# Kernel optimization log

Measured on AMD Instinct MI355X. Metric: run time of the kernel, lower is better.

Reference implementation:

```python
import jax, jax.numpy as jnp
import numpy as np

EPS = 1e-12  # F.normalize eps


def _lstm_dir(x, Wih_d, Whh_d, b_d, reverse):
    # x: [M, dim]; Wih_d/Whh_d: [4*dim, dim]; b_d: [4*dim]
    dim = Whh_d.shape[1]
    def step(carry, xt):
        h, c = carry
        z = xt @ Wih_d.T + h @ Whh_d.T + b_d  # [4*dim]
        i, f, g, o = jnp.split(z, 4)
        i = jax.nn.sigmoid(i); f = jax.nn.sigmoid(f)
        g = jnp.tanh(g); o = jax.nn.sigmoid(o)
        c = f * c + i * g
        h = o * jnp.tanh(c)
        return (h, c), h
    init = (jnp.zeros((dim,), x.dtype), jnp.zeros((dim,), x.dtype))
    _, hs = jax.lax.scan(step, init, x, reverse=reverse)
    return hs  # [M, dim]


def _forward(fingerprints, adjacency, words, emb_fp, emb_word,
             Wg, bg, Wih, Whh, bih, bhh, Wc, bc, Wp, bp, Wo, bo, Wi, bi):
    # ---- GAT over compound graph ----
    xs = emb_fp[fingerprints]  # [N, dim]
    L_gat = Wg.shape[0]
    for i in range(L_gat):
        hs = jax.nn.relu(xs @ Wg[i].T + bg[i])          # [N, dim]
        w = hs @ hs.T                                    # [N, N]
        attn = w * adjacency
        denom = jnp.maximum(jnp.sum(jnp.abs(attn), axis=1, keepdims=True), EPS)
        xs = xs + (attn / denom) @ hs
    x = xs  # compound atom vectors [N, dim]

    # ---- bidirectional LSTM over protein words ----
    wv = emb_word[words]  # [M, dim]
    h_f = _lstm_dir(wv, Wih[0], Whh[0], bih[0] + bhh[0], reverse=False)
    h_b = _lstm_dir(wv, Wih[1], Whh[1], bih[1] + bhh[1], reverse=True)
    xs_rnn = jax.nn.relu(jnp.concatenate([h_f, h_b], axis=1))  # [M, 2*dim]

    # ---- cross attention pooling ----
    h = jax.nn.relu(x @ Wc.T + bc)         # [N, dim]
    hp = jax.nn.relu(xs_rnn @ Wp.T + bp)   # [M, dim]
    weights = h @ hp.T                     # [N, M]
    w_comp = jnp.mean(weights, axis=1)     # [N]  (mean over M)
    w_prot = jnp.mean(weights, axis=0)     # [M]
    y = w_comp[:, None] * h                # [N, dim]
    ys = w_prot[:, None] * hp              # [M, dim]
    compound_vector = jnp.mean(y, axis=0)[None, :]   # [1, dim]
    protein_vector = jnp.mean(ys, axis=0)[None, :]   # [1, dim]

    # ---- output MLP ----
    cat = jnp.concatenate([compound_vector, protein_vector], axis=1)  # [1, 2*dim]
    L_out = Wo.shape[0]
    for j in range(L_out):
        cat = jax.nn.relu(cat @ Wo[j].T + bo[j])
    interaction = cat @ Wi.T + bi  # [1, 2]
    return interaction, weights


def setup_inputs() -> dict:
    key = jax.random.key(0)
    ks = jax.random.split(key, 16)
    N, M, DIM = 4096, 4096, 128
    N_FP, N_WORD = 100000, 10000
    L_GAT, L_OUT = 3, 2
    s = 0.05
    return {
        "fingerprints": jax.random.randint(ks[0], (N,), 0, N_FP),
        "adjacency": jax.random.uniform(ks[1], (N, N), jnp.float32),
        "words": jax.random.randint(ks[2], (M,), 0, N_WORD),
        "emb_fp": jax.random.normal(ks[3], (N_FP, DIM), jnp.float32) * s,
        "emb_word": jax.random.normal(ks[4], (N_WORD, DIM), jnp.float32) * s,
        "Wg": jax.random.normal(ks[5], (L_GAT, DIM, DIM), jnp.float32) * s,
        "bg": jnp.zeros((L_GAT, DIM), jnp.float32),
        "Wih": jax.random.normal(ks[6], (2, 4 * DIM, DIM), jnp.float32) * s,
        "Whh": jax.random.normal(ks[7], (2, 4 * DIM, DIM), jnp.float32) * s,
        "bih": jnp.zeros((2, 4 * DIM), jnp.float32),
        "bhh": jnp.zeros((2, 4 * DIM), jnp.float32),
        "Wc": jax.random.normal(ks[8], (DIM, DIM), jnp.float32) * s,
        "bc": jnp.zeros((DIM,), jnp.float32),
        "Wp": jax.random.normal(ks[9], (DIM, 2 * DIM), jnp.float32) * s,
        "bp": jnp.zeros((DIM,), jnp.float32),
        "Wo": jax.random.normal(ks[10], (L_OUT, 2 * DIM, 2 * DIM), jnp.float32) * s,
        "bo": jnp.zeros((L_OUT, 2 * DIM), jnp.float32),
        "Wi": jax.random.normal(ks[11], (2, 2 * DIM), jnp.float32) * s,
        "bi": jnp.zeros((2,), jnp.float32),
    }


def reference(fingerprints, adjacency, words, emb_fp, emb_word,
              Wg, bg, Wih, Whh, bih, bhh, Wc, bc, Wp, bp, Wo, bo, Wi, bi):
    return _forward(fingerprints, adjacency, words, emb_fp, emb_word,
                    Wg, bg, Wih, Whh, bih, bhh, Wc, bc, Wp, bp, Wo, bo, Wi, bi)
```

## Files before the change

### kernel.cpp

```cpp
#include <hip/hip_runtime.h>
#include <hip/hip_bf16.h>
#include <math.h>

#define DIM 128

typedef float v2f __attribute__((ext_vector_type(2)));
typedef _Float16 v2h __attribute__((ext_vector_type(2)));
typedef _Float16 h8v __attribute__((ext_vector_type(8)));
typedef short s8v __attribute__((ext_vector_type(8)));
typedef float f4v __attribute__((ext_vector_type(4)));

template<int CTRL>
__device__ inline float dpp_movf(float v) {
  int x = __builtin_amdgcn_update_dpp(0, __float_as_int(v), CTRL, 0xF, 0xF, true);
  return __int_as_float(x);
}
template<int CTRL>
__device__ inline float dpp_xadd(float v) { return v + dpp_movf<CTRL>(v); }

__device__ inline float dot8u(uint4 a, uint4 b, float acc) {
#if __has_builtin(__builtin_amdgcn_fdot2)
  acc = __builtin_amdgcn_fdot2(__builtin_bit_cast(v2h, a.x), __builtin_bit_cast(v2h, b.x), acc, false);
  acc = __builtin_amdgcn_fdot2(__builtin_bit_cast(v2h, a.y), __builtin_bit_cast(v2h, b.y), acc, false);
  acc = __builtin_amdgcn_fdot2(__builtin_bit_cast(v2h, a.z), __builtin_bit_cast(v2h, b.z), acc, false);
  acc = __builtin_amdgcn_fdot2(__builtin_bit_cast(v2h, a.w), __builtin_bit_cast(v2h, b.w), acc, false);
#else
  const v2h* pa = (const v2h*)&a; const v2h* pb = (const v2h*)&b;
#pragma unroll
  for (int i = 0; i < 4; ++i) {
    acc += (float)pa[i][0] * (float)pb[i][0];
    acc += (float)pa[i][1] * (float)pb[i][1];
  }
#endif
  return acc;
}

__device__ inline unsigned pk2h(float a, float b) {
  return __builtin_bit_cast(unsigned, __builtin_amdgcn_cvt_pkrtz(a, b));
}
__device__ inline float sigm_fast(float z) {
  return __builtin_amdgcn_rcpf(1.f + __expf(-z));
}
__device__ inline float tanh_fast(float z) {
  float e = __expf(-2.f * z);
  return (1.f - e) * __builtin_amdgcn_rcpf(1.f + e);
}
__device__ inline ushort f2bf(float x) {
  unsigned u = __builtin_bit_cast(unsigned, x);
  return (ushort)((u + 0x7FFFu + ((u >> 16) & 1u)) >> 16);
}
__device__ inline unsigned pk2bf(float a, float b) {
  return (unsigned)f2bf(a) | ((unsigned)f2bf(b) << 16);
}

__global__ void gather_rows(const float* __restrict__ table, const int* __restrict__ idx,
                            float* __restrict__ dst, int n) {
  int i = blockIdx.x * blockDim.x + threadIdx.x;
  int total = n * 32;
  if (i >= total) return;
  int r = i >> 5, c = i & 31;
  const float4* src = (const float4*)table + (size_t)idx[r] * 32 + c;
  ((float4*)dst)[i] = *src;
}
__global__ void gather_rows_wv(const float* __restrict__ table, const int* __restrict__ idx,
                               float* __restrict__ dst, _Float16* __restrict__ dsth, int n) {
  int i = blockIdx.x * blockDim.x + threadIdx.x;
  int total = n * 32;
  if (i >= total) return;
  int r = i >> 5, c = i & 31;
  float4 v = ((const float4*)table)[(size_t)idx[r] * 32 + c];
  ((float4*)dst)[i] = v;
  ((uint2*)dsth)[i] = make_uint2(pk2h(v.x, v.y), pk2h(v.z, v.w));
}

__global__ void conv_f16(const float* __restrict__ src, _Float16* __restrict__ dst, int n4) {
  int i = blockIdx.x * blockDim.x + threadIdx.x;
  if (i >= n4) return;
  float4 v = ((const float4*)src)[i];
  ((uint2*)dst)[i] = make_uint2(pk2h(v.x, v.y), pk2h(v.z, v.w));
}

__global__ void tr_bf16(const ushort* __restrict__ src, ushort* __restrict__ dT, int n) {
  int i = blockIdx.x * blockDim.x + threadIdx.x;
  if (i >= n * DIM) return;
  int r = i >> 7, d = i & 127;
  dT[(size_t)d * n + r] = src[i];
}

template<bool RELU, int OM>
__global__ __launch_bounds__(256) void gemm_nt(
    const float* __restrict__ A, const float* __restrict__ B,
    float* __restrict__ C, ushort* __restrict__ Cb, _Float16* __restrict__ Ch,
    int ldc, int K, const float* __restrict__ bias)
{
  __shared__ float As[64][17];
  __shared__ float Bs[64][17];
  int tid = threadIdx.x;
  int tx = tid & 15, ty = tid >> 4;
  int rowBase = blockIdx.y * 64, colBase = blockIdx.x * 64;
  int lr = tid >> 2, lk = (tid & 3) * 4;
  float acc[4][4] = {};
  for (int k0 = 0; k0 < K; k0 += 16) {
    float4 av = *(const float4*)&A[(size_t)(rowBase + lr) * K + k0 + lk];
    float4 bv = *(const float4*)&B[(size_t)(colBase + lr) * K + k0 + lk];
    As[lr][lk+0]=av.x; As[lr][lk+1]=av.y; As[lr][lk+2]=av.z; As[lr][lk+3]=av.w;
    Bs[lr][lk+0]=bv.x; Bs[lr][lk+1]=bv.y; Bs[lr][lk+2]=bv.z; Bs[lr][lk+3]=bv.w;
    __syncthreads();
#pragma unroll
    for (int kk = 0; kk < 16; ++kk) {
      float a0=As[ty*4+0][kk], a1=As[ty*4+1][kk], a2=As[ty*4+2][kk], a3=As[ty*4+3][kk];
      float b0=Bs[tx*4+0][kk], b1=Bs[tx*4+1][kk], b2=Bs[tx*4+2][kk], b3=Bs[tx*4+3][kk];
      acc[0][0]+=a0*b0; acc[0][1]+=a0*b1; acc[0][2]+=a0*b2; acc[0][3]+=a0*b3;
      acc[1][0]+=a1*b0; acc[1][1]+=a1*b1; acc[1][2]+=a1*b2; acc[1][3]+=a1*b3;
      acc[2][0]+=a2*b0; acc[2][1]+=a2*b1; acc[2][2]+=a2*b2; acc[2][3]+=a2*b3;
      acc[3][0]+=a3*b0; acc[3][1]+=a3*b1; acc[3][2]+=a3*b2; acc[3][3]+=a3*b3;
    }
    __syncthreads();
  }
  int row = rowBase + ty*4, col = colBase + tx*4;
#pragma unroll
  for (int i = 0; i < 4; ++i) {
    float v[4];
#pragma unroll
    for (int j = 0; j < 4; ++j) {
      float x = acc[i][j] + bias[col + j];
      if (RELU) x = fmaxf(x, 0.f);
      v[j] = x;
    }
    size_t base = (size_t)(row + i) * ldc + col;
    if (OM == 1) {
      *(uint2*)&Cb[base] = make_uint2(pk2bf(v[0], v[1]), pk2bf(v[2], v[3]));
    } else {
      float* cp = &C[base];
      *(float2*)cp = make_float2(v[0], v[1]);
      *(float2*)(cp+2) = make_float2(v[2], v[3]);
      if (OM == 2)
        *(uint2*)&Ch[base] = make_uint2(pk2h(v[0], v[1]), pk2h(v[2], v[3]));
    }
  }
}

#define LDT 136
__global__ __launch_bounds__(256) void mfma_nt_adj(
    const ushort* __restrict__ A, const ushort* __restrict__ B,
    ushort* __restrict__ C, int ldc,
    const float* __restrict__ adj, int ldadj)
{
  __shared__ ushort As[128][LDT];
  __shared__ ushort Bs[128][LDT];
  int tid = threadIdx.x;
  int rowBase = blockIdx.y * 128, colBase = blockIdx.x * 128;
#pragma unroll
  for (int it = 0; it < 8; ++it) {
    int c = it * 256 + tid;
    int r = c >> 4, ch = (c & 15) * 8;
    *(uint4*)&As[r][ch] = *(const uint4*)&A[(size_t)(rowBase + r) * DIM + ch];
    *(uint4*)&Bs[r][ch] = *(const uint4*)&B[(size_t)(colBase + r) * DIM + ch];
  }
  __syncthreads();
  int lane = tid & 63;
  int wv = tid >> 6, wr = wv >> 1, wc = wv & 1;
  int lr = lane & 15, lk = (lane >> 4) * 8;
  f4v acc[4][4] = {};
#pragma unroll
  for (int kc = 0; kc < 4; ++kc) {
    s8v a[4], b[4];
#pragma unroll
    for (int i = 0; i < 4; ++i) {
      a[i] = *(const s8v*)&As[wr*64 + i*16 + lr][kc*32 + lk];
      b[i] = *(const s8v*)&Bs[wc*64 + i*16 + lr][kc*32 + lk];
    }
#pragma unroll
    for (int i = 0; i < 4; ++i)
#pragma unroll
      for (int j = 0; j < 4; ++j)
        acc[i][j] = __builtin_amdgcn_mfma_f32_16x16x32_bf16(a[i], b[j], acc[i][j], 0, 0, 0);
  }
  int rsub = (lane >> 4) * 4;
#pragma unroll
  for (int i = 0; i < 4; ++i)
#pragma unroll
    for (int j = 0; j < 4; ++j) {
      int col = colBase + wc*64 + j*16 + lr;
#pragma unroll
      for (int rg = 0; rg < 4; ++rg) {
        int row = rowBase + wr*64 + i*16 + rsub + rg;
        float v = acc[i][j][rg] * adj[(size_t)row * ldadj + col];
        C[(size_t)row * ldc + col] = f2bf(v);
      }
    }
}

__global__ __launch_bounds__(256) void mfma_nt_f32(
    const _Float16* __restrict__ A, const _Float16* __restrict__ B,
    float* __restrict__ C, int ldc)
{
  __shared__ ushort As[128][LDT];
  __shared__ ushort Bs[128][LDT];
  int tid = threadIdx.x;
  int rowBase = blockIdx.y * 128, colBase = blockIdx.x * 128;
#pragma unroll
  for (int it = 0; it < 8; ++it) {
    int c = it * 256 + tid;
    int r = c >> 4, ch = (c & 15) * 8;
    *(uint4*)&As[r][ch] = *(const uint4*)&A[(size_t)(rowBase + r) * DIM + ch];
    *(uint4*)&Bs[r][ch] = *(const uint4*)&B[(size_t)(colBase + r) * DIM + ch];
  }
  __syncthreads();
  int lane = tid & 63;
  int wv = tid >> 6, wr = wv >> 1, wc = wv & 1;
  int lr = lane & 15, lk = (lane >> 4) * 8;
  f4v acc[4][4] = {};
#pragma unroll
  for (int kc = 0; kc < 4; ++kc) {
    h8v a[4], b[4];
#pragma unroll
    for (int i = 0; i < 4; ++i) {
      a[i] = *(const h8v*)&As[wr*64 + i*16 + lr][kc*32 + lk];
      b[i] = *(const h8v*)&Bs[wc*64 + i*16 + lr][kc*32 + lk];
    }
#pragma unroll
    for (int i = 0; i < 4; ++i)
#pragma unroll
      for (int j = 0; j < 4; ++j)
        acc[i][j] = __builtin_amdgcn_mfma_f32_16x16x32_f16(a[i], b[j], acc[i][j], 0, 0, 0);
  }
  int rsub = (lane >> 4) * 4;
#pragma unroll
  for (int i = 0; i < 4; ++i)
#pragma unroll
    for (int j = 0; j < 4; ++j) {
      int col = colBase + wc*64 + j*16 + lr;
#pragma unroll
      for (int rg = 0; rg < 4; ++rg) {
        int row = rowBase + wr*64 + i*16 + rsub + rg;
        C[(size_t)row * ldc + col] = acc[i][j][rg];
      }
    }
}

__global__ __launch_bounds__(256) void mfma_wx(
    const _Float16* __restrict__ A,
    const _Float16* __restrict__ Bw,
    const float* __restrict__ bias,
    float* __restrict__ out)
{
  __shared__ ushort As[128][LDT];
  __shared__ ushort Bs[128][LDT];
  int tid = threadIdx.x;
  int m0 = blockIdx.y * 128, colBase = blockIdx.x * 128;
#pragma unroll
  for (int it = 0; it < 8; ++it) {
    int c = it * 256 + tid;
    int r = c >> 4, ch = (c & 15) * 8;
    *(uint4*)&As[r][ch] = *(const uint4*)&A[(size_t)(m0 + r) * DIM + ch];
    int j = colBase + r;
    int brow = 128 * (j & 3) + (j >> 2);
    *(uint4*)&Bs[r][ch] = *(const uint4*)&Bw[(size_t)brow * DIM + ch];
  }
  __syncthreads();
  int lane = tid & 63;
  int wv = tid >> 6, wr = wv >> 1, wc = wv & 1;
  int lr = lane & 15, lk = (lane >> 4) * 8;
  f4v acc[4][4] = {};
#pragma unroll
  for (int kc = 0; kc < 4; ++kc) {
    h8v a[4], b[4];
#pragma unroll
    for (int i = 0; i < 4; ++i) {
      a[i] = *(const h8v*)&As[wr*64 + i*16 + lr][kc*32 + lk];
      b[i] = *(const h8v*)&Bs[wc*64 + i*16 + lr][kc*32 + lk];
    }
#pragma unroll
    for (int i = 0; i < 4; ++i)
#pragma unroll
      for (int j = 0; j < 4; ++j)
        acc[i][j] = __builtin_amdgcn_mfma_f32_16x16x32_f16(a[i], b[j], acc[i][j], 0, 0, 0);
  }
  int rsub = (lane >> 4) * 4;
#pragma unroll
  for (int i = 0; i < 4; ++i)
#pragma unroll
    for (int j = 0; j < 4; ++j) {
      int col = colBase + wc*64 + j*16 + lr;
      int brow = 128 * (col & 3) + (col >> 2);
      float bv = bias[brow];
#pragma unroll
      for (int rg = 0; rg < 4; ++rg) {
        int row = m0 + wr*64 + i*16 + rsub + rg;
        out[(size_t)row * 512 + col] = acc[i][j][rg] + bv;
      }
    }
}

#define LDT2 72
__global__ __launch_bounds__(256) void mfma_av(
    const ushort* __restrict__ attnb, const ushort* __restrict__ hsT,
    float* __restrict__ pt, int chunk, int N)
{
  __shared__ ushort As[128][LDT2];
  __shared__ ushort Bs[128][LDT2];
  int tid = threadIdx.x;
  int n0 = blockIdx.x * 128;
  int m0 = blockIdx.y * chunk;
  int lane = tid & 63;
  int wv = tid >> 6, wr = wv >> 1, wc = wv & 1;
  int lr = lane & 15, lk = (lane >> 4) * 8;
  f4v acc[4][4] = {};
  for (int mt = 0; mt < chunk; mt += 64) {
#pragma unroll
    for (int it = 0; it < 4; ++it) {
      int c = it * 256 + tid;
      int r = c >> 3, ch = (c & 7) * 8;
      *(uint4*)&As[r][ch] = *(const uint4*)&attnb[(size_t)(n0 + r) * N + m0 + mt + ch];
      *(uint4*)&Bs[r][ch] = *(const uint4*)&hsT[(size_t)r * N + m0 + mt + ch];
    }
    __syncthreads();
#pragma unroll
    for (int kc = 0; kc < 2; ++kc) {
      s8v a[4], b[4];
#pragma unroll
      for (int i = 0; i < 4; ++i) {
        a[i] = *(const s8v*)&As[wr*64 + i*16 + lr][kc*32 + lk];
        b[i] = *(const s8v*)&Bs[wc*64 + i*16 + lr][kc*32 + lk];
      }
#pragma unroll
      for (int i = 0; i < 4; ++i)
#pragma unroll
        for (int j = 0; j < 4; ++j)
          acc[i][j] = __builtin_amdgcn_mfma_f32_16x16x32_bf16(a[i], b[j], acc[i][j], 0, 0, 0);
    }
    __syncthreads();
  }
  size_t base = ((size_t)blockIdx.y * N + n0) * DIM;
  int rsub = (lane >> 4) * 4;
#pragma unroll
  for (int i = 0; i < 4; ++i)
#pragma unroll
    for (int j = 0; j < 4; ++j) {
      int d = wc*64 + j*16 + lr;
#pragma unroll
      for (int rg = 0; rg < 4; ++rg) {
        int nn = wr*64 + i*16 + rsub + rg;
        pt[base + (size_t)nn * DIM + d] = acc[i][j][rg];
      }
    }
}

__global__ void row_reduce_abs_bf16(const ushort* __restrict__ W, int ld, int M,
                                    float* __restrict__ out, float eps) {
  int n = blockIdx.x;
  const ushort* row = W + (size_t)n * ld;
  float s = 0;
  for (int m = threadIdx.x * 8; m < M; m += 256 * 8) {
    uint4 v = *(const uint4*)&row[m];
    unsigned a[4] = {v.x, v.y, v.z, v.w};
#pragma unroll
    for (int q = 0; q < 4; ++q) {
      s += __int_as_float((int)((a[q] & 0x7FFFu) << 16));
      s += __int_as_float((int)(a[q] & 0x7FFF0000u));
    }
  }
  __shared__ float red[256];
  red[threadIdx.x] = s; __syncthreads();
  for (int k = 128; k > 0; k >>= 1) {
    if (threadIdx.x < k) red[threadIdx.x] += red[threadIdx.x + k];
    __syncthreads();
  }
  if (threadIdx.x == 0) out[n] = fmaxf(red[0], eps);
}

__global__ void row_mean(const float* __restrict__ W, int ld, int M,
                         float* __restrict__ out, float inv) {
  int n = blockIdx.x;
  const float* row = W + (size_t)n * ld;
  float s = 0;
  for (int m = threadIdx.x; m < M; m += 256) s += row[m];
  __shared__ float red[256];
  red[threadIdx.x] = s; __syncthreads();
  for (int k = 128; k > 0; k >>= 1) {
    if (threadIdx.x < k) red[threadIdx.x] += red[threadIdx.x + k];
    __syncthreads();
  }
  if (threadIdx.x == 0) out[n] = red[0] * inv;
}

__global__ void colmean_part(const float* __restrict__ W, int ld, int rows_per,
                             float* __restrict__ part, int M) {
  int m = blockIdx.x * blockDim.x + threadIdx.x;
  int n0 = blockIdx.y * rows_per;
  float s = 0;
  for (int n = 0; n < rows_per; ++n) s += W[(size_t)(n0 + n) * ld + m];
  part[(size_t)blockIdx.y * M + m] = s;
}
__global__ void colmean_fin(const float* __restrict__ part, int M, int nparts,
                            float* __restrict__ out, float inv) {
  int m = blockIdx.x * blockDim.x + threadIdx.x;
  float s = 0;
  for (int k = 0; k < nparts; ++k) s += part[(size_t)k * M + m];
  out[m] = s * inv;
}

__global__ void axpy_reduce(const float* __restrict__ pt, const float* __restrict__ denom,
                            float* __restrict__ xs, int total) {
  int i = blockIdx.x * blockDim.x + threadIdx.x;
  if (i >= total) return;
  float s = 0;
#pragma unroll
  for (int k = 0; k < 8; ++k) s += pt[(size_t)k * total + i];
  xs[i] += s / denom[i >> 7];
}

__global__ void add_vec(const float* __restrict__ a, const float* __restrict__ b,
                        float* __restrict__ o, int n) {
  int i = blockIdx.x * blockDim.x + threadIdx.x;
  if (i < n) o[i] = a[i] + b[i];
}

__global__ __launch_bounds__(512, 2) void lstm_kernel(
    const float* __restrict__ Whh,
    const float* __restrict__ Wxp,
    float* __restrict__ xs_rnn,
    int M)
{
  int dir = blockIdx.x;
  int tid = threadIdx.x;
  int w = tid >> 6, lane = tid & 63;
  int u  = w * 16 + (lane >> 2);
  int gp = (lane >> 1) & 1;
  int kh = lane & 1;
  int row0 = gp ? (256 + u) : u;
  const float* base = Whh + (size_t)dir * 512 * DIM;
  const float4* w0p = (const float4*)(base + (size_t)row0 * DIM + kh * 64);
  const float4* w1p = (const float4*)(base + (size_t)(row0 + 128) * DIM + kh * 64);

#define REP8(X) X(0) X(1) X(2) X(3) X(4) X(5) X(6) X(7)
#define DECLW(r) uint4 wA##r, wB##r;
  REP8(DECLW)
#define LOADW(r) { \
    float4 x = w0p[2*(r)], y = w0p[2*(r)+1]; \
    wA##r = make_uint4(pk2h(x.x,x.y), pk2h(x.z,x.w), pk2h(y.x,y.y), pk2h(y.z,y.w)); \
    x = w1p[2*(r)]; y = w1p[2*(r)+1]; \
    wB##r = make_uint4(pk2h(x.x,x.y), pk2h(x.z,x.w), pk2h(y.x,y.y), pk2h(y.z,y.w)); }
  REP8(LOADW)

  __shared__ __align__(16) _Float16 hbuf[2][DIM];
  if (tid < DIM) hbuf[0][tid] = (_Float16)0.f;
  float c = 0.f;
  __syncthreads();

  const float* WxD = Wxp + (size_t)dir * M * 512;
  int wxcol = 4 * u + 2 * gp;
  int t0 = dir ? (M - 1) : 0;
  float2 wx = *(const float2*)&WxD[(size_t)t0 * 512 + wxcol];
  for (int s = 0; s < M; ++s) {
    int t = dir ? (M - 1 - s) : s;
    float2 wxn = make_float2(0.f, 0.f);
    if (s + 1 < M) {
      int tn = dir ? (M - 2 - s) : (s + 1);
      wxn = *(const float2*)&WxD[(size_t)tn * 512 + wxcol];
    }
    int cur = s & 1;
    const uint4* hb = (const uint4*)(hbuf[cur]) + kh * 8;
    float a00 = 0.f, a01 = 0.f, a02 = 0.f, a03 = 0.f;
    float a10 = 0.f, a11 = 0.f, a12 = 0.f, a13 = 0.f;
    {
      uint4 h0 = hb[0], h1 = hb[1], h2 = hb[2], h3 = hb[3];
      uint4 h4 = hb[4], h5 = hb[5], h6 = hb[6], h7 = hb[7];
      a00 = dot8u(wA0, h0, a00); a10 = dot8u(wB0, h0, a10);
      a01 = dot8u(wA1, h1, a01); a11 = dot8u(wB1, h1, a11);
      a02 = dot8u(wA2, h2, a02); a12 = dot8u(wB2, h2, a12);
      a03 = dot8u(wA3, h3, a03); a13 = dot8u(wB3, h3, a13);
      a00 = dot8u(wA4, h4, a00); a10 = dot8u(wB4, h4, a10);
      a01 = dot8u(wA5, h5, a01); a11 = dot8u(wB5, h5, a11);
      a02 = dot8u(wA6, h6, a02); a12 = dot8u(wB6, h6, a12);
      a03 = dot8u(wA7, h7, a03); a13 = dot8u(wB7, h7, a13);
    }
    float a0 = (a00 + a01) + (a02 + a03);
    float a1 = (a10 + a11) + (a12 + a13);
    float z0 = dpp_xadd<0xB1>(a0) + wx.x;
    float z1 = dpp_xadd<0xB1>(a1) + wx.y;
    float av0 = gp ? tanh_fast(z0) : sigm_fast(z0);
    float av1 = sigm_fast(z1);
    float gv = dpp_movf<0x102>(av0);
    float ov = dpp_movf<0x102>(av1);
    if ((lane & 3) == 0) {
      c = av1 * c + av0 * gv;
      float hv = ov * tanh_fast(c);
      hbuf[cur ^ 1][u] = (_Float16)hv;
      xs_rnn[(size_t)t * (2 * DIM) + dir * DIM + u] = fmaxf(hv, 0.f);
    }
    wx = wxn;
    __syncthreads();
  }
#undef LOADW
#undef DECLW
#undef REP8
}

__global__ void pool_vec(const float* __restrict__ mat, const float* __restrict__ wv,
                         int n, float* __restrict__ out, float inv) {
  int t = threadIdx.x; int g = t >> 7, d = t & 127;
  float acc = 0;
  for (int r = g; r < n; r += 8) acc += wv[r] * mat[(size_t)r * DIM + d];
  __shared__ float red[1024];
  red[t] = acc; __syncthreads();
  if (g == 0) {
    float s = acc;
#pragma unroll
    for (int k = 1; k < 8; ++k) s += red[k * 128 + d];
    out[d] = s * inv;
  }
}

__global__ void mlp_kernel(const float* __restrict__ cvec, const float* __restrict__ pvec,
                           const float* __restrict__ Wo, const float* __restrict__ bo,
                           const float* __restrict__ Wi, const float* __restrict__ bi,
                           float* __restrict__ out) {
  __shared__ float buf0[256], buf1[256];
  int t = threadIdx.x;
  buf0[t] = (t < 128) ? cvec[t] : pvec[t - 128];
  __syncthreads();
  {
    const float* W = Wo;
    float s = bo[t];
    for (int v = 0; v < 256; ++v) s += W[t * 256 + v] * buf0[v];
    buf1[t] = fmaxf(s, 0.f);
  }
  __syncthreads();
  {
    const float* W = Wo + 256 * 256;
    float s = bo[256 + t];
    for (int v = 0; v < 256; ++v) s += W[t * 256 + v] * buf1[v];
    buf0[t] = fmaxf(s, 0.f);
  }
  __syncthreads();
  if (t < 2) {
    float s = bi[t];
    for (int v = 0; v < 256; ++v) s += Wi[t * 256 + v] * buf0[v];
    out[t] = s;
  }
}

extern "C" void kernel_launch(void* const* d_in, const int* in_sizes, int n_in,
                              void* d_out, int out_size, void* d_ws, size_t ws_size,
                              hipStream_t stream) {
  const int*   fingerprints = (const int*)d_in[0];
  const float* adjacency    = (const float*)d_in[1];
  const int*   words        = (const int*)d_in[2];
  const float* emb_fp       = (const float*)d_in[3];
  const float* emb_word     = (const float*)d_in[4];
  const float* Wg  = (const float*)d_in[5];
  const float* bg  = (const float*)d_in[6];
  const float* Wih = (const float*)d_in[7];
  const float* Whh = (const float*)d_in[8];
  const float* bih = (const float*)d_in[9];
  const float* bhh = (const float*)d_in[10];
  const float* Wc  = (const float*)d_in[11];
  const float* bc  = (const float*)d_in[12];
  const float* Wp  = (const float*)d_in[13];
  const float* bp  = (const float*)d_in[14];
  const float* Wo  = (const float*)d_in[15];
  const float* bo  = (const float*)d_in[16];
  const float* Wi  = (const float*)d_in[17];
  const float* bi  = (const float*)d_in[18];

  const int N = in_sizes[0];
  const int M = in_sizes[2];
  const int LGAT = in_sizes[5] / (DIM * DIM);

  float* out  = (float*)d_out;
  float* attn = out + 2;
  ushort* attnb = (ushort*)attn;

  float* ws = (float*)d_ws;
  size_t off = 0;
  auto alloc = [&](size_t nf) { float* p = ws + off; off += (nf + 3) & ~(size_t)3; return p; };
  float* xs     = alloc((size_t)N * DIM);
  float* wvb    = alloc((size_t)M * DIM);
  float* denom  = alloc(N);
  float* pt     = alloc((size_t)8 * N * DIM);
  float* Wx     = pt;
  float* xs_rnn = alloc((size_t)M * 2 * DIM);
  float* hp     = alloc((size_t)M * DIM);
  float* hmat   = alloc((size_t)N * DIM);
  float* bsum   = alloc(1024);
  float* wcomp  = alloc(N);
  float* wprot  = alloc(M);
  float* cvec   = alloc(DIM);
  float* pvec   = alloc(DIM);
  float* cpart  = alloc((size_t)32 * M);
  ushort* hs_b  = (ushort*)alloc((size_t)N * DIM / 2);
  ushort* hsT_b = (ushort*)alloc((size_t)N * DIM / 2);
  _Float16* wvb_h  = (_Float16*)alloc((size_t)M * DIM / 2);
  _Float16* wih_h  = (_Float16*)alloc((size_t)2 * 512 * DIM / 2);
  _Float16* hmat_h = (_Float16*)alloc((size_t)N * DIM / 2);
  _Float16* hp_h   = (_Float16*)alloc((size_t)M * DIM / 2);
  (void)ws_size; (void)n_in; (void)out_size;

  gather_rows<<<(N * 32 + 255) / 256, 256, 0, stream>>>(emb_fp, fingerprints, xs, N);
  gather_rows_wv<<<(M * 32 + 255) / 256, 256, 0, stream>>>(emb_word, words, wvb, wvb_h, M);

  for (int l = 0; l < LGAT; ++l) {
    gemm_nt<true, 1><<<dim3(DIM / 64, N / 64), 256, 0, stream>>>(
        xs, Wg + (size_t)l * DIM * DIM, nullptr, hs_b, nullptr, DIM, DIM, bg + l * DIM);
    tr_bf16<<<(N * DIM) / 256, 256, 0, stream>>>(hs_b, hsT_b, N);
    mfma_nt_adj<<<dim3(N / 128, N / 128), 256, 0, stream>>>(
        hs_b, hs_b, attnb, N, adjacency, N);
    row_reduce_abs_bf16<<<N, 256, 0, stream>>>(attnb, N, N, denom, 1e-12f);
    mfma_av<<<dim3(N / 128, 8), 256, 0, stream>>>(attnb, hsT_b, pt, N / 8, N);
    axpy_reduce<<<(N * DIM) / 256, 256, 0, stream>>>(pt, denom, xs, N * DIM);
  }

  add_vec<<<4, 256, 0, stream>>>(bih, bhh, bsum, 1024);
  conv_f16<<<(2 * 512 * DIM / 4 + 255) / 256, 256, 0, stream>>>(Wih, wih_h, 2 * 512 * DIM / 4);
  for (int d = 0; d < 2; ++d) {
    mfma_wx<<<dim3(512 / 128, M / 128), 256, 0, stream>>>(
        wvb_h, wih_h + (size_t)d * 512 * DIM, bsum + d * 512, Wx + (size_t)d * M * 512);
  }
  lstm_kernel<<<2, 512, 0, stream>>>(Whh, Wx, xs_rnn, M);

  gemm_nt<true, 2><<<dim3(DIM / 64, M / 64), 256, 0, stream>>>(
      xs_rnn, Wp, hp, nullptr, hp_h, DIM, 2 * DIM, bp);
  gemm_nt<true, 2><<<dim3(DIM / 64, N / 64), 256, 0, stream>>>(
      xs, Wc, hmat, nullptr, hmat_h, DIM, DIM, bc);
  mfma_nt_f32<<<dim3(M / 128, N / 128), 256, 0, stream>>>(hmat_h, hp_h, attn, M);
  row_mean<<<N, 256, 0, stream>>>(attn, M, M, wcomp, 1.f / (float)M);
  colmean_part<<<dim3(M / 256, 32), 256, 0, stream>>>(attn, M, N / 32, cpart, M);
  colmean_fin<<<M / 256, 256, 0, stream>>>(cpart, M, 32, wprot, 1.f / (float)N);
  pool_vec<<<1, 1024, 0, stream>>>(hmat, wcomp, N, cvec, 1.f / (float)N);
  pool_vec<<<1, 1024, 0, stream>>>(hp, wprot, M, pvec, 1.f / (float)M);

  mlp_kernel<<<1, 256, 0, stream>>>(cvec, pvec, Wo, bo, Wi, bi, out);
}
```

Before: 3.178 ms.

## Split pooling across blocks, widen MLP kernel, simplify LSTM dot accumulation

```diff
diff --git a/kernel.cpp b/kernel.cpp
--- a/kernel.cpp
+++ b/kernel.cpp
@@ -240,10 +240,8 @@
 }
 
 __global__ __launch_bounds__(256) void mfma_wx(
-    const _Float16* __restrict__ A,
-    const _Float16* __restrict__ Bw,
-    const float* __restrict__ bias,
-    float* __restrict__ out)
+    const _Float16* __restrict__ A, const _Float16* __restrict__ Bw,
+    const float* __restrict__ bias, float* __restrict__ out)
 {
   __shared__ ushort As[128][LDT];
   __shared__ ushort Bs[128][LDT];
@@ -416,6 +414,8 @@
   int i = blockIdx.x * blockDim.x + threadIdx.x;
   if (i < n) o[i] = a[i] + b[i];
 }
+
+#define REP8(X) X(0) X(1) X(2) X(3) X(4) X(5) X(6) X(7)
 
 __global__ __launch_bounds__(512, 2) void lstm_kernel(
     const float* __restrict__ Whh,
@@ -434,7 +434,6 @@
   const float4* w0p = (const float4*)(base + (size_t)row0 * DIM + kh * 64);
   const float4* w1p = (const float4*)(base + (size_t)(row0 + 128) * DIM + kh * 64);
 
-#define REP8(X) X(0) X(1) X(2) X(3) X(4) X(5) X(6) X(7)
 #define DECLW(r) uint4 wA##r, wB##r;
   REP8(DECLW)
 #define LOADW(r) { \
@@ -462,22 +461,9 @@
     }
     int cur = s & 1;
     const uint4* hb = (const uint4*)(hbuf[cur]) + kh * 8;
-    float a00 = 0.f, a01 = 0.f, a02 = 0.f, a03 = 0.f;
-    float a10 = 0.f, a11 = 0.f, a12 = 0.f, a13 = 0.f;
-    {
-      uint4 h0 = hb[0], h1 = hb[1], h2 = hb[2], h3 = hb[3];
-      uint4 h4 = hb[4], h5 = hb[5], h6 = hb[6], h7 = hb[7];
-      a00 = dot8u(wA0, h0, a00); a10 = dot8u(wB0, h0, a10);
-      a01 = dot8u(wA1, h1, a01); a11 = dot8u(wB1, h1, a11);
-      a02 = dot8u(wA2, h2, a02); a12 = dot8u(wB2, h2, a12);
-      a03 = dot8u(wA3, h3, a03); a13 = dot8u(wB3, h3, a13);
-      a00 = dot8u(wA4, h4, a00); a10 = dot8u(wB4, h4, a10);
-      a01 = dot8u(wA5, h5, a01); a11 = dot8u(wB5, h5, a11);
-      a02 = dot8u(wA6, h6, a02); a12 = dot8u(wB6, h6, a12);
-      a03 = dot8u(wA7, h7, a03); a13 = dot8u(wB7, h7, a13);
-    }
-    float a0 = (a00 + a01) + (a02 + a03);
-    float a1 = (a10 + a11) + (a12 + a13);
+    float a0 = 0.f, a1 = 0.f;
+#define DOTW(r) { uint4 hv = hb[r]; a0 = dot8u(wA##r, hv, a0); a1 = dot8u(wB##r, hv, a1); }
+    REP8(DOTW)
     float z0 = dpp_xadd<0xB1>(a0) + wx.x;
     float z1 = dpp_xadd<0xB1>(a1) + wx.y;
     float av0 = gp ? tanh_fast(z0) : sigm_fast(z0);
@@ -493,24 +479,33 @@
     wx = wxn;
     __syncthreads();
   }
+#undef DOTW
 #undef LOADW
 #undef DECLW
 #undef REP8
 }
 
-__global__ void pool_vec(const float* __restrict__ mat, const float* __restrict__ wv,
-                         int n, float* __restrict__ out, float inv) {
+__global__ void pool_part(const float* __restrict__ mat, const float* __restrict__ wv,
+                          int chunk, float* __restrict__ part) {
   int t = threadIdx.x; int g = t >> 7, d = t & 127;
+  int r0 = blockIdx.x * chunk;
   float acc = 0;
-  for (int r = g; r < n; r += 8) acc += wv[r] * mat[(size_t)r * DIM + d];
+  for (int r = g; r < chunk; r += 8) acc += wv[r0 + r] * mat[(size_t)(r0 + r) * DIM + d];
   __shared__ float red[1024];
   red[t] = acc; __syncthreads();
   if (g == 0) {
     float s = acc;
 #pragma unroll
     for (int k = 1; k < 8; ++k) s += red[k * 128 + d];
-    out[d] = s * inv;
-  }
+    part[(size_t)blockIdx.x * DIM + d] = s;
+  }
+}
+__global__ void pool_fin(const float* __restrict__ part, int nparts,
+                         float* __restrict__ out, float inv) {
+  int d = threadIdx.x;
+  float s = 0;
+  for (int k = 0; k < nparts; ++k) s += part[(size_t)k * DIM + d];
+  out[d] = s * inv;
 }
 
 __global__ void mlp_kernel(const float* __restrict__ cvec, const float* __restrict__ pvec,
@@ -518,28 +513,41 @@
                            const float* __restrict__ Wi, const float* __restrict__ bi,
                            float* __restrict__ out) {
   __shared__ float buf0[256], buf1[256];
+  __shared__ float red[1024];
   int t = threadIdx.x;
-  buf0[t] = (t < 128) ? cvec[t] : pvec[t - 128];
+  int nr = t >> 2, part = t & 3;
+  if (t < 128) buf0[t] = cvec[t];
+  else if (t < 256) buf0[t] = pvec[t - 128];
   __syncthreads();
   {
-    const float* W = Wo;
-    float s = bo[t];
-    for (int v = 0; v < 256; ++v) s += W[t * 256 + v] * buf0[v];
-    buf1[t] = fmaxf(s, 0.f);
+    const float* W = Wo + (size_t)nr * 256 + part * 64;
+    const float* x = buf0 + part * 64;
+    float s = 0;
+    for (int v = 0; v < 64; ++v) s += W[v] * x[v];
+    red[t] = s; __syncthreads();
+    if (part == 0) buf1[nr] = fmaxf(red[t] + red[t+1] + red[t+2] + red[t+3] + bo[nr], 0.f);
   }
   __syncthreads();
   {
-    const float* W = Wo + 256 * 256;
-    float s = bo[256 + t];
-    for (int v = 0; v < 256; ++v) s += W[t * 256 + v] * buf1[v];
-    buf0[t] = fmaxf(s, 0.f);
-  }
-  __syncthreads();
-  if (t < 2) {
-    float s = bi[t];
-    for (int v = 0; v < 256; ++v) s += Wi[t * 256 + v] * buf0[v];
-    out[t] = s;
-  }
+    const float* W = Wo + 256 * 256 + (size_t)nr * 256 + part * 64;
+    const float* x = buf1 + part * 64;
+    float s = 0;
+    for (int v = 0; v < 64; ++v) s += W[v] * x[v];
+    red[t] = s; __syncthreads();
+    if (part == 0) buf0[nr] = fmaxf(red[t] + red[t+1] + red[t+2] + red[t+3] + bo[256 + nr], 0.f);
+  }
+  __syncthreads();
+  if (t < 8) {
+    int o = t >> 2, p = t & 3;
+    const float* W = Wi + (size_t)o * 256 + p * 64;
+    const float* x = buf0 + p * 64;
+    float s = 0;
+    for (int v = 0; v < 64; ++v) s += W[v] * x[v];
+    red[t] = s;
+  }
+  __syncthreads();
+  if (t < 2)
+    out[t] = red[4*t] + red[4*t+1] + red[4*t+2] + red[4*t+3] + bi[t];
 }
 
 extern "C" void kernel_launch(void* const* d_in, const int* in_sizes, int n_in,
@@ -590,6 +598,7 @@
   float* cvec   = alloc(DIM);
   float* pvec   = alloc(DIM);
   float* cpart  = alloc((size_t)32 * M);
+  float* ppart  = alloc((size_t)16 * DIM);
   ushort* hs_b  = (ushort*)alloc((size_t)N * DIM / 2);
   ushort* hsT_b = (ushort*)alloc((size_t)N * DIM / 2);
   _Float16* wvb_h  = (_Float16*)alloc((size_t)M * DIM / 2);
@@ -628,8 +637,10 @@
   row_mean<<<N, 256, 0, stream>>>(attn, M, M, wcomp, 1.f / (float)M);
   colmean_part<<<dim3(M / 256, 32), 256, 0, stream>>>(attn, M, N / 32, cpart, M);
   colmean_fin<<<M / 256, 256, 0, stream>>>(cpart, M, 32, wprot, 1.f / (float)N);
-  pool_vec<<<1, 1024, 0, stream>>>(hmat, wcomp, N, cvec, 1.f / (float)N);
-  pool_vec<<<1, 1024, 0, stream>>>(hp, wprot, M, pvec, 1.f / (float)M);
-
-  mlp_kernel<<<1, 256, 0, stream>>>(cvec, pvec, Wo, bo, Wi, bi, out);
-}
+  pool_part<<<16, 1024, 0, stream>>>(hmat, wcomp, N / 16, ppart);
+  pool_fin<<<1, DIM, 0, stream>>>(ppart, 16, cvec, 1.f / (float)N);
+  pool_part<<<16, 1024, 0, stream>>>(hp, wprot, M / 16, ppart);
+  pool_fin<<<1, DIM, 0, stream>>>(ppart, 16, pvec, 1.f / (float)M);
+
+  mlp_kernel<<<1, 1024, 0, stream>>>(cvec, pvec, Wo, bo, Wi, bi, out);
+}
```

New measurement: 2.675 ms (median of 2 runs). 1.19x faster.
